# Kernel optimization log

Hardware: AMD Instinct MI355X
Metric: run time of the kernel (lower is better)

The kernel has to match this reference:

```python
import jax, jax.numpy as jnp
from jax import lax
import numpy as np

B, T, C = 32, 1024, 512
K = 3
MAX_DUR = 4            # durations drawn from [0,5) -> max value 4
L_MAX = T * MAX_DUR    # static padded mel length (torch pads to batch max; we pad to static max)
EPS = 1e-5


def conv_ln_block(x, w, b, g, beta):
    # x: [B,T,C]; torch ConvLNBlock: permute -> Conv1d(SAME) -> relu -> permute -> LayerNorm -> dropout(eval=id)
    y = lax.conv_general_dilated(x.transpose(0, 2, 1), w, (1,), 'SAME',
                                 dimension_numbers=('NCH', 'OIH', 'NCH')) + b[None, :, None]
    y = jax.nn.relu(y).transpose(0, 2, 1)  # [B,T,Cout]
    mu = y.mean(-1, keepdims=True)
    var = y.var(-1, keepdims=True)
    return (y - mu) * lax.rsqrt(var + EPS) * g + beta


def regulate(batch, durations, token_lengths):
    # Vectorized equivalent of DurationRegulator.inflate: repeat token t durations[b,t] times,
    # concatenate, pad. Implemented as cumsum + searchsorted gather (single pass, no ragged loops).
    pos = jnp.arange(T)
    valid = pos[None, :] < token_lengths[:, None]          # [B,T]
    d = jnp.where(valid, durations, 0)
    total = d.sum(axis=1)
    # torch: if durs.sum()==0 -> fill with 1
    d = jnp.where((total == 0)[:, None], valid.astype(d.dtype), d)
    total = d.sum(axis=1)                                   # [B]
    cum = jnp.cumsum(d, axis=1)                             # inclusive cumsum [B,T]
    frames = jnp.arange(L_MAX)
    idx = jax.vmap(lambda c: jnp.searchsorted(c, frames, side='right'))(cum)  # [B,L_MAX]
    idx = jnp.clip(idx, 0, T - 1)
    out = jnp.take_along_axis(batch, idx[:, :, None], axis=1)                 # [B,L_MAX,C]
    frame_mask = frames[None, :] < total[:, None]
    out = out * frame_mask[:, :, None].astype(batch.dtype)
    return out, total.astype(jnp.float32)


def setup_inputs() -> dict:
    key = jax.random.key(0)
    ks = jax.random.split(key, 8)
    batch = jax.random.normal(ks[0], (B, T, C), dtype=jnp.float32)
    token_lengths = jax.random.randint(ks[1], (B,), T // 2, T + 1).astype(jnp.int32)
    mask = jnp.arange(T)[None, :] < token_lengths[:, None]
    label_durations = jax.random.randint(ks[2], (B, T), 0, MAX_DUR + 1).astype(jnp.int32)
    s1 = 1.0 / np.sqrt(C * K)
    s2 = 1.0 / np.sqrt(C * K)
    params = {
        'conv1_w': jax.random.uniform(ks[3], (C, C, K), minval=-s1, maxval=s1, dtype=jnp.float32),
        'conv1_b': jnp.zeros((C,), jnp.float32),
        'ln1_g': jnp.ones((C,), jnp.float32), 'ln1_b': jnp.zeros((C,), jnp.float32),
        'conv2_w': jax.random.uniform(ks[4], (C, C, K), minval=-s2, maxval=s2, dtype=jnp.float32),
        'conv2_b': jnp.zeros((C,), jnp.float32),
        'ln2_g': jnp.ones((C,), jnp.float32), 'ln2_b': jnp.zeros((C,), jnp.float32),
        'lin_w': jax.random.uniform(ks[5], (C, 1), minval=-1/np.sqrt(C), maxval=1/np.sqrt(C), dtype=jnp.float32),
        'lin_b': jnp.zeros((1,), jnp.float32),
    }
    return dict(batch=batch, token_lengths=token_lengths, mask=mask,
                label_durations=label_durations, **params)


def reference(batch, token_lengths, mask, label_durations,
              conv1_w, conv1_b, ln1_g, ln1_b,
              conv2_w, conv2_b, ln2_g, ln2_b,
              lin_w, lin_b):
    # VariancePredictor: two ConvLN blocks + Linear(out_channels, 1), masked fill 0
    h = conv_ln_block(batch, conv1_w, conv1_b, ln1_g, ln1_b)
    h = conv_ln_block(h, conv2_w, conv2_b, ln2_g, ln2_b)
    predicted_durations = h @ lin_w + lin_b                      # [B,T,1]
    predicted_durations = jnp.where(mask[:, :, None], predicted_durations, 0.0)
    # label_durations provided -> regulator uses labels (training path), alpha=1
    padded_batch, mel_lengths = regulate(batch, label_durations, token_lengths)
    return padded_batch, mel_lengths, predicted_durations
```

## Files before the change

### kernel.cpp

```cpp
#include <hip/hip_runtime.h>
#include <hip/hip_bf16.h>
#include <stdint.h>


typedef _Float16 f16;
typedef _Float16 f16x8 __attribute__((ext_vector_type(8)));
typedef float f32x4 __attribute__((ext_vector_type(4)));

#define B_    32
#define T_    1024
#define TP_   1026
#define C_    512
#define LMAX_ 4096
#define KDIM  1536

#define XPAD_OFF   0u
#define H1PAD_OFF  33619968u
#define W1T_OFF    67239936u
#define W2T_OFF    68812800u
#define YWS_OFF    70385664u
#define TOT_OFF    137494528u
#define IDX_OFF    137495040u
#define GWL_OFF    138019328u
#define K12_OFF    138021376u
#define STAT2_OFF  138021888u

#define AS1C(p) ((const __attribute__((address_space(1))) void*)(p))
#define AS3(p)  ((__attribute__((address_space(3))) void*)(p))

#define PP_BLOCKS   2052
#define PW_BLOCKS   256
#define SCAN_BLOCKS 32

__global__ __launch_bounds__(1024) void fused_prep(
        const float* __restrict__ batch, f16* __restrict__ xpad,
        f16* __restrict__ h1pad, const int* __restrict__ tlen,
        const float* __restrict__ w1, const float* __restrict__ w2,
        f16* __restrict__ w1t, f16* __restrict__ w2t,
        const float* __restrict__ g2, const float* __restrict__ be2,
        const float* __restrict__ lw, float* __restrict__ gwl,
        float* __restrict__ k12,
        const int* __restrict__ dur, int* __restrict__ idxarr,
        int* __restrict__ total, float* __restrict__ mel_out) {
    __shared__ int sd[1024];
    __shared__ int sv[1024];
    __shared__ float rk[8][2];
    const int bid = blockIdx.x;
    const int tid = threadIdx.x;

    if (bid < PP_BLOCKS) {
        int row = bid * 16 + (tid >> 6);
        int lane = tid & 63;
        int b = row / TP_, tt = row % TP_;
        size_t dsto = (size_t)row * C_ + lane * 8;
        if (tt == 0 || tt == TP_ - 1) {
            f16x8 z = {};
            *(f16x8*)(xpad + dsto) = z;
            *(f16x8*)(h1pad + dsto) = z;
        } else if (tt <= tlen[b] + 130) {
            const float* src = batch + ((size_t)(b * T_ + tt - 1)) * C_ + lane * 8;
            float4 v0 = ((const float4*)src)[0];
            float4 v1 = ((const float4*)src)[1];
            f16x8 h;
            h[0] = (f16)v0.x; h[1] = (f16)v0.y; h[2] = (f16)v0.z; h[3] = (f16)v0.w;
            h[4] = (f16)v1.x; h[5] = (f16)v1.y; h[6] = (f16)v1.z; h[7] = (f16)v1.w;
            *(f16x8*)(xpad + dsto) = h;
        }
        return;
    }
    if (bid < PP_BLOCKS + PW_BLOCKS) {
        int unit = (bid - PP_BLOCKS) * 4 + (tid >> 8);
        int o = unit & 511;
        const float* w = (unit >> 9) ? w2 : w1;
        f16* wt = (unit >> 9) ? w2t : w1t;
        int tl = tid & 255;
        for (int j = tl; j < KDIM; j += 256) {
            int tap = j >> 9, i = j & 511;
            wt[(size_t)o * KDIM + j] = (f16)w[(size_t)o * KDIM + i * 3 + tap];
        }
        return;
    }
    if (bid < PP_BLOCKS + PW_BLOCKS + SCAN_BLOCKS) {
        int b = bid - (PP_BLOCKS + PW_BLOCKS);
        int t = tid;
        int L = tlen[b];
        int valid = (t < L) ? 1 : 0;
        int d = valid ? dur[b * T_ + t] : 0;
        sd[t] = d; sv[t] = valid;
        __syncthreads();
        for (int off = 1; off < 1024; off <<= 1) {
            int x = 0, y = 0;
            if (t >= off) { x = sd[t - off]; y = sv[t - off]; }
            __syncthreads();
            sd[t] += x; sv[t] += y;
            __syncthreads();
        }
        int totd = sd[1023];
        int cur  = (totd == 0) ? sv[t] : sd[t];
        int prev = (t == 0) ? 0 : ((totd == 0) ? sv[t - 1] : sd[t - 1]);
        for (int f = prev; f < cur; f++) idxarr[b * LMAX_ + f] = t;
        if (t == 1023) {
            int tt = (totd == 0) ? sv[1023] : totd;
            total[b] = tt;
            mel_out[b] = (float)tt;
        }
        return;
    }
    {
        float k1 = 0.f, k2 = 0.f;
        if (tid < C_) {
            float gw_ = g2[tid] * lw[tid];
            gwl[tid] = gw_;
            k1 = gw_;
            k2 = be2[tid] * lw[tid];
        }
#pragma unroll
        for (int m = 32; m; m >>= 1) {
            k1 += __shfl_xor(k1, m, 64);
            k2 += __shfl_xor(k2, m, 64);
        }
        int wv = tid >> 6;
        if ((tid & 63) == 0 && wv < 8) { rk[wv][0] = k1; rk[wv][1] = k2; }
        __syncthreads();
        if (tid == 0) {
            float a1 = 0.f, a2 = 0.f;
#pragma unroll
            for (int i = 0; i < 8; i++) { a1 += rk[i][0]; a2 += rk[i][1]; }
            k12[0] = a1; k12[1] = a2;
        }
    }
}

template<int EPI>
__global__ __launch_bounds__(256, 2) void gemm_k(const f16* __restrict__ A,
                                                 const f16* __restrict__ Bw,
                                                 const float* __restrict__ bias,
                                                 f16* __restrict__ Y,
                                                 const float* __restrict__ gwl,
                                                 float4* __restrict__ stats,
                                                 const int* __restrict__ tlen) {
    __shared__ f16 As[128 * 64];
    __shared__ f16 Bs[256 * 64];
    const int m0 = blockIdx.x * 128;
    {
        const int bb = m0 >> 10, t0 = m0 & 1023;
        const int L = tlen[bb];
        if (EPI == 0 ? (t0 > L) : (t0 >= L)) return;
    }
    const int tid = threadIdx.x;
    const int lane = tid & 63;
    const int w = tid >> 6;
    const int n0 = blockIdx.y * 256;
    const int arow0 = (m0 >> 10) * TP_ + (m0 & 1023);
    const int wm = (w & 1) * 64;
    const int wn = (w >> 1) * 128;

    f32x4 acc[4][8];
#pragma unroll
    for (int i = 0; i < 4; i++)
#pragma unroll
        for (int j = 0; j < 8; j++) acc[i][j] = (f32x4){0.f, 0.f, 0.f, 0.f};

    const int lrow = lane >> 3;
    const int gran = (lane & 7) ^ lrow;
    const f16* aB = A + (size_t)(arow0 + lrow) * C_ + gran * 8;
    const f16* bB = Bw + (size_t)(n0 + lrow) * KDIM + gran * 8;

    for (int kk = 0; kk < KDIM; kk += 64) {
        __syncthreads();
#pragma unroll
        for (int i = 0; i < 4; i++) {
            const int rb = (w + i * 4) * 8;
            __builtin_amdgcn_global_load_lds(AS1C(aB + (size_t)rb * C_ + kk),
                                             AS3(&As[rb * 64]), 16, 0, 0);
        }
#pragma unroll
        for (int j = 0; j < 8; j++) {
            const int rb = (w + j * 4) * 8;
            __builtin_amdgcn_global_load_lds(AS1C(bB + (size_t)rb * KDIM + kk),
                                             AS3(&Bs[rb * 64]), 16, 0, 0);
        }
        __syncthreads();
#pragma unroll
        for (int ks = 0; ks < 2; ks++) {
            const int sl = ((ks << 2) + (lane >> 4)) ^ (lane & 7);
            f16x8 af[4], bf[8];
#pragma unroll
            for (int mi = 0; mi < 4; mi++)
                af[mi] = *(const f16x8*)&As[(wm + mi * 16 + (lane & 15)) * 64 + sl * 8];
#pragma unroll
            for (int ni = 0; ni < 8; ni++)
                bf[ni] = *(const f16x8*)&Bs[(wn + ni * 16 + (lane & 15)) * 64 + sl * 8];
#pragma unroll
            for (int mi = 0; mi < 4; mi++)
#pragma unroll
                for (int ni = 0; ni < 8; ni++)
                    acc[mi][ni] = __builtin_amdgcn_mfma_f32_16x16x32_f16(
                        af[mi], bf[ni], acc[mi][ni], 0, 0, 0);
        }
    }

    const int col = lane & 15;
    const int row4 = (lane >> 4) * 4;

    if (EPI == 0) {
#pragma unroll
        for (int ni = 0; ni < 8; ni++) {
            int n = n0 + wn + ni * 16 + col;
            float bn = bias[n];
#pragma unroll
            for (int mi = 0; mi < 4; mi++) {
#pragma unroll
                for (int r = 0; r < 4; r++) {
                    int m = m0 + wm + mi * 16 + row4 + r;
                    float v = acc[mi][ni][r] + bn;
                    Y[(size_t)m * C_ + n] = (f16)(v > 0.f ? v : 0.f);
                }
            }
        }
    } else {
        float bn[8], gw[8];
#pragma unroll
        for (int ni = 0; ni < 8; ni++) {
            int n = n0 + wn + ni * 16 + col;
            bn[ni] = bias[n];
            gw[ni] = gwl[n];
        }
        float s_[4][4], q_[4][4], u_[4][4];
#pragma unroll
        for (int mi = 0; mi < 4; mi++)
#pragma unroll
            for (int r = 0; r < 4; r++) { s_[mi][r] = 0.f; q_[mi][r] = 0.f; u_[mi][r] = 0.f; }
#pragma unroll
        for (int mi = 0; mi < 4; mi++)
#pragma unroll
            for (int ni = 0; ni < 8; ni++)
#pragma unroll
                for (int r = 0; r < 4; r++) {
                    float v = acc[mi][ni][r] + bn[ni];
                    v = v > 0.f ? v : 0.f;
                    s_[mi][r] += v;
                    q_[mi][r] += v * v;
                    u_[mi][r] += v * gw[ni];
                }
#pragma unroll
        for (int m = 8; m; m >>= 1)
#pragma unroll
            for (int mi = 0; mi < 4; mi++)
#pragma unroll
                for (int r = 0; r < 4; r++) {
                    s_[mi][r] += __shfl_xor(s_[mi][r], m, 64);
                    q_[mi][r] += __shfl_xor(q_[mi][r], m, 64);
                    u_[mi][r] += __shfl_xor(u_[mi][r], m, 64);
                }
        __syncthreads();
        float* red = (float*)As;
        if (col == 0) {
#pragma unroll
            for (int mi = 0; mi < 4; mi++)
#pragma unroll
                for (int r = 0; r < 4; r++) {
                    int row = wm + mi * 16 + row4 + r;
                    int idx = ((w >> 1) * 128 + row) * 3;
                    red[idx]     = s_[mi][r];
                    red[idx + 1] = q_[mi][r];
                    red[idx + 2] = u_[mi][r];
                }
        }
        __syncthreads();
        if (tid < 128) {
            float S = red[tid * 3]     + red[(128 + tid) * 3];
            float Q = red[tid * 3 + 1] + red[(128 + tid) * 3 + 1];
            float U = red[tid * 3 + 2] + red[(128 + tid) * 3 + 2];
            stats[(size_t)(m0 + tid) * 2 + blockIdx.y] = (float4){S, Q, U, 0.f};
        }
    }
}

__global__ __launch_bounds__(256) void ln_kernel(const f16* __restrict__ Y,
                                                 const float* __restrict__ g,
                                                 const float* __restrict__ be,
                                                 f16* __restrict__ hpad,
                                                 const int* __restrict__ tlen) {
    int row = blockIdx.x * 4 + (threadIdx.x >> 6);
    int lane = threadIdx.x & 63;
    int b = row >> 10, t = row & 1023;
    if (t > tlen[b]) return;
    f16x8 yv = *(const f16x8*)(Y + (size_t)row * C_ + lane * 8);
    float v[8];
#pragma unroll
    for (int i = 0; i < 8; i++) v[i] = (float)yv[i];
    float s = 0.f, q = 0.f;
#pragma unroll
    for (int i = 0; i < 8; i++) { s += v[i]; q += v[i] * v[i]; }
#pragma unroll
    for (int m = 32; m; m >>= 1) { s += __shfl_xor(s, m, 64); q += __shfl_xor(q, m, 64); }
    float mu = s * (1.f / 512.f);
    float x = q * (1.f / 512.f) - mu * mu + 1e-5f;
    float rs = rsqrtf(x);
    rs = rs * (1.5f - 0.5f * x * rs * rs);
    const float4 g0 = ((const float4*)g)[lane * 2], g1 = ((const float4*)g)[lane * 2 + 1];
    const float4 e0 = ((const float4*)be)[lane * 2], e1 = ((const float4*)be)[lane * 2 + 1];
    f16x8 h;
    h[0] = (f16)((v[0] - mu) * rs * g0.x + e0.x);
    h[1] = (f16)((v[1] - mu) * rs * g0.y + e0.y);
    h[2] = (f16)((v[2] - mu) * rs * g0.z + e0.z);
    h[3] = (f16)((v[3] - mu) * rs * g0.w + e0.w);
    h[4] = (f16)((v[4] - mu) * rs * g1.x + e1.x);
    h[5] = (f16)((v[5] - mu) * rs * g1.y + e1.y);
    h[6] = (f16)((v[6] - mu) * rs * g1.z + e1.z);
    h[7] = (f16)((v[7] - mu) * rs * g1.w + e1.w);
    *(f16x8*)(hpad + ((size_t)(b * TP_ + t + 1)) * C_ + lane * 8) = h;
}

__global__ __launch_bounds__(256) void gather_fin(const float* __restrict__ batch,
                                                  const int* __restrict__ idxarr,
                                                  const int* __restrict__ total,
                                                  float* __restrict__ out,
                                                  const float4* __restrict__ stats,
                                                  const float* __restrict__ k12,
                                                  const float* __restrict__ lb,
                                                  const int* __restrict__ tlen,
                                                  float* __restrict__ pred) {
    if (blockIdx.x < 32768) {
        int gw = blockIdx.x * 4 + (threadIdx.x >> 6);
        int lane = threadIdx.x & 63;
        int b = gw >> 12;
        int l = gw & (LMAX_ - 1);
        int tot = total[b];
        float4* dst = (float4*)(out + ((size_t)b * LMAX_ + l) * C_);
        if (l < tot) {
            int idx = idxarr[gw];
            const float4* src = (const float4*)(batch + ((size_t)b * T_ + idx) * C_);
            dst[lane] = src[lane];
            dst[lane + 64] = src[lane + 64];
        } else {
            float4 z = {0.f, 0.f, 0.f, 0.f};
            dst[lane] = z;
            dst[lane + 64] = z;
        }
    } else {
        int m = (blockIdx.x - 32768) * 256 + threadIdx.x;
        float4 a = stats[(size_t)m * 2];
        float4 b = stats[(size_t)m * 2 + 1];
        float S = a.x + b.x, Q = a.y + b.y, U = a.z + b.z;
        float mu = S * (1.f / 512.f);
        float x = Q * (1.f / 512.f) - mu * mu + 1e-5f;
        float rs = rsqrtf(x);
        rs = rs * (1.5f - 0.5f * x * rs * rs);
        float p = rs * (U - mu * k12[0]) + k12[1] + lb[0];
        int bb = m >> 10, t = m & 1023;
        pred[m] = (t < tlen[bb]) ? p : 0.f;
    }
}

extern "C" void kernel_launch(void* const* d_in, const int* in_sizes, int n_in,
                              void* d_out, int out_size, void* d_ws, size_t ws_size,
                              hipStream_t stream) {
    const float* batch = (const float*)d_in[0];
    const int* tlen    = (const int*)d_in[1];
    const int* durs    = (const int*)d_in[3];
    const float* w1  = (const float*)d_in[4];
    const float* b1  = (const float*)d_in[5];
    const float* g1  = (const float*)d_in[6];
    const float* be1 = (const float*)d_in[7];
    const float* w2  = (const float*)d_in[8];
    const float* b2  = (const float*)d_in[9];
    const float* g2  = (const float*)d_in[10];
    const float* be2 = (const float*)d_in[11];
    const float* lw  = (const float*)d_in[12];
    const float* lb  = (const float*)d_in[13];

    float* out      = (float*)d_out;
    float* mel_out  = out + (size_t)B_ * LMAX_ * C_;
    float* pred_out = mel_out + B_;

    char* ws    = (char*)d_ws;
    f16* xpad   = (f16*)(ws + XPAD_OFF);
    f16* h1pad  = (f16*)(ws + H1PAD_OFF);
    f16* w1t    = (f16*)(ws + W1T_OFF);
    f16* w2t    = (f16*)(ws + W2T_OFF);
    f16* yws    = (f16*)(ws + YWS_OFF);
    int* tot    = (int*)(ws + TOT_OFF);
    int* idxarr = (int*)(ws + IDX_OFF);
    float* gwl  = (float*)(ws + GWL_OFF);
    float* k12  = (float*)(ws + K12_OFF);
    float4* st2 = (float4*)(ws + STAT2_OFF);

    fused_prep<<<PP_BLOCKS + PW_BLOCKS + SCAN_BLOCKS + 1, 1024, 0, stream>>>(
        batch, xpad, h1pad, tlen, w1, w2, w1t, w2t,
        g2, be2, lw, gwl, k12, durs, idxarr, tot, mel_out);
    gemm_k<0><<<dim3(256, 2), 256, 0, stream>>>(xpad, w1t, b1, yws,
                                                nullptr, nullptr, tlen);
    ln_kernel<<<8192, 256, 0, stream>>>(yws, g1, be1, h1pad, tlen);
    gemm_k<1><<<dim3(256, 2), 256, 0, stream>>>(h1pad, w2t, b2, nullptr,
                                                gwl, st2, tlen);
    gather_fin<<<32768 + 128, 256, 0, stream>>>(batch, idxarr, tot, out,
                                                st2, k12, lb, tlen, pred_out);
}
```

Measured before the change: 450.2 us.

## Fuse mel gather into LN kernel and move scan blocks first in prep

Moves the large regulator gather (copying batch rows into the padded mel output) out of the final kernel and into the layer-norm kernel, so it runs in the same launch as LN1, between the two GEMMs. The prediction finalize becomes its own small kernel. The scan blocks are reordered to the front of the prep grid so the index array is produced early. The aim is to hide the memory-bound gather alongside LN work. The risk is that the gather's bandwidth use now competes with LN and delays the second GEMM.

New measurement: 460.8 us. +2.4%, slower.

```diff
diff --git a/kernel.cpp b/kernel.cpp
--- a/kernel.cpp
+++ b/kernel.cpp
@@ -28,9 +28,12 @@
 #define AS1C(p) ((const __attribute__((address_space(1))) void*)(p))
 #define AS3(p)  ((__attribute__((address_space(3))) void*)(p))
 
+#define SCAN_BLOCKS 32
 #define PP_BLOCKS   2052
 #define PW_BLOCKS   256
-#define SCAN_BLOCKS 32
+
+#define LN_BLOCKS   8192
+#define GA_BLOCKS   32768
 
 __global__ __launch_bounds__(1024) void fused_prep(
         const float* __restrict__ batch, f16* __restrict__ xpad,
@@ -48,8 +51,34 @@
     const int bid = blockIdx.x;
     const int tid = threadIdx.x;
 
-    if (bid < PP_BLOCKS) {
-        int row = bid * 16 + (tid >> 6);
+    if (bid < SCAN_BLOCKS) {
+        int b = bid;
+        int t = tid;
+        int L = tlen[b];
+        int valid = (t < L) ? 1 : 0;
+        int d = valid ? dur[b * T_ + t] : 0;
+        sd[t] = d; sv[t] = valid;
+        __syncthreads();
+        for (int off = 1; off < 1024; off <<= 1) {
+            int x = 0, y = 0;
+            if (t >= off) { x = sd[t - off]; y = sv[t - off]; }
+            __syncthreads();
+            sd[t] += x; sv[t] += y;
+            __syncthreads();
+        }
+        int totd = sd[1023];
+        int cur  = (totd == 0) ? sv[t] : sd[t];
+        int prev = (t == 0) ? 0 : ((totd == 0) ? sv[t - 1] : sd[t - 1]);
+        for (int f = prev; f < cur; f++) idxarr[b * LMAX_ + f] = t;
+        if (t == 1023) {
+            int tt = (totd == 0) ? sv[1023] : totd;
+            total[b] = tt;
+            mel_out[b] = (float)tt;
+        }
+        return;
+    }
+    if (bid < SCAN_BLOCKS + PP_BLOCKS) {
+        int row = (bid - SCAN_BLOCKS) * 16 + (tid >> 6);
         int lane = tid & 63;
         int b = row / TP_, tt = row % TP_;
         size_t dsto = (size_t)row * C_ + lane * 8;
@@ -68,8 +97,8 @@
         }
         return;
     }
-    if (bid < PP_BLOCKS + PW_BLOCKS) {
-        int unit = (bid - PP_BLOCKS) * 4 + (tid >> 8);
+    if (bid < SCAN_BLOCKS + PP_BLOCKS + PW_BLOCKS) {
+        int unit = (bid - SCAN_BLOCKS - PP_BLOCKS) * 4 + (tid >> 8);
         int o = unit & 511;
         const float* w = (unit >> 9) ? w2 : w1;
         f16* wt = (unit >> 9) ? w2t : w1t;
@@ -77,32 +106,6 @@
         for (int j = tl; j < KDIM; j += 256) {
             int tap = j >> 9, i = j & 511;
             wt[(size_t)o * KDIM + j] = (f16)w[(size_t)o * KDIM + i * 3 + tap];
-        }
-        return;
-    }
-    if (bid < PP_BLOCKS + PW_BLOCKS + SCAN_BLOCKS) {
-        int b = bid - (PP_BLOCKS + PW_BLOCKS);
-        int t = tid;
-        int L = tlen[b];
-        int valid = (t < L) ? 1 : 0;
-        int d = valid ? dur[b * T_ + t] : 0;
-        sd[t] = d; sv[t] = valid;
-        __syncthreads();
-        for (int off = 1; off < 1024; off <<= 1) {
-            int x = 0, y = 0;
-            if (t >= off) { x = sd[t - off]; y = sv[t - off]; }
-            __syncthreads();
-            sd[t] += x; sv[t] += y;
-            __syncthreads();
-        }
-        int totd = sd[1023];
-        int cur  = (totd == 0) ? sv[t] : sd[t];
-        int prev = (t == 0) ? 0 : ((totd == 0) ? sv[t - 1] : sd[t - 1]);
-        for (int f = prev; f < cur; f++) idxarr[b * LMAX_ + f] = t;
-        if (t == 1023) {
-            int tt = (totd == 0) ? sv[1023] : totd;
-            total[b] = tt;
-            mel_out[b] = (float)tt;
         }
         return;
     }
@@ -277,54 +280,44 @@
     }
 }
 
-__global__ __launch_bounds__(256) void ln_kernel(const f16* __restrict__ Y,
-                                                 const float* __restrict__ g,
-                                                 const float* __restrict__ be,
-                                                 f16* __restrict__ hpad,
-                                                 const int* __restrict__ tlen) {
-    int row = blockIdx.x * 4 + (threadIdx.x >> 6);
-    int lane = threadIdx.x & 63;
-    int b = row >> 10, t = row & 1023;
-    if (t > tlen[b]) return;
-    f16x8 yv = *(const f16x8*)(Y + (size_t)row * C_ + lane * 8);
-    float v[8];
-#pragma unroll
-    for (int i = 0; i < 8; i++) v[i] = (float)yv[i];
-    float s = 0.f, q = 0.f;
-#pragma unroll
-    for (int i = 0; i < 8; i++) { s += v[i]; q += v[i] * v[i]; }
-#pragma unroll
-    for (int m = 32; m; m >>= 1) { s += __shfl_xor(s, m, 64); q += __shfl_xor(q, m, 64); }
-    float mu = s * (1.f / 512.f);
-    float x = q * (1.f / 512.f) - mu * mu + 1e-5f;
-    float rs = rsqrtf(x);
-    rs = rs * (1.5f - 0.5f * x * rs * rs);
-    const float4 g0 = ((const float4*)g)[lane * 2], g1 = ((const float4*)g)[lane * 2 + 1];
-    const float4 e0 = ((const float4*)be)[lane * 2], e1 = ((const float4*)be)[lane * 2 + 1];
-    f16x8 h;
-    h[0] = (f16)((v[0] - mu) * rs * g0.x + e0.x);
-    h[1] = (f16)((v[1] - mu) * rs * g0.y + e0.y);
-    h[2] = (f16)((v[2] - mu) * rs * g0.z + e0.z);
-    h[3] = (f16)((v[3] - mu) * rs * g0.w + e0.w);
-    h[4] = (f16)((v[4] - mu) * rs * g1.x + e1.x);
-    h[5] = (f16)((v[5] - mu) * rs * g1.y + e1.y);
-    h[6] = (f16)((v[6] - mu) * rs * g1.z + e1.z);
-    h[7] = (f16)((v[7] - mu) * rs * g1.w + e1.w);
-    *(f16x8*)(hpad + ((size_t)(b * TP_ + t + 1)) * C_ + lane * 8) = h;
-}
-
-__global__ __launch_bounds__(256) void gather_fin(const float* __restrict__ batch,
-                                                  const int* __restrict__ idxarr,
-                                                  const int* __restrict__ total,
-                                                  float* __restrict__ out,
-                                                  const float4* __restrict__ stats,
-                                                  const float* __restrict__ k12,
-                                                  const float* __restrict__ lb,
-                                                  const int* __restrict__ tlen,
-                                                  float* __restrict__ pred) {
-    if (blockIdx.x < 32768) {
-        int gw = blockIdx.x * 4 + (threadIdx.x >> 6);
-        int lane = threadIdx.x & 63;
+__global__ __launch_bounds__(256) void ln_gather(
+        const f16* __restrict__ Y, const float* __restrict__ g,
+        const float* __restrict__ be, f16* __restrict__ hpad,
+        const int* __restrict__ tlen,
+        const float* __restrict__ batch, const int* __restrict__ idxarr,
+        const int* __restrict__ total, float* __restrict__ out) {
+    const int lane = threadIdx.x & 63;
+    if (blockIdx.x < LN_BLOCKS) {
+        int row = blockIdx.x * 4 + (threadIdx.x >> 6);
+        int b = row >> 10, t = row & 1023;
+        if (t > tlen[b]) return;
+        f16x8 yv = *(const f16x8*)(Y + (size_t)row * C_ + lane * 8);
+        float v[8];
+#pragma unroll
+        for (int i = 0; i < 8; i++) v[i] = (float)yv[i];
+        float s = 0.f, q = 0.f;
+#pragma unroll
+        for (int i = 0; i < 8; i++) { s += v[i]; q += v[i] * v[i]; }
+#pragma unroll
+        for (int m = 32; m; m >>= 1) { s += __shfl_xor(s, m, 64); q += __shfl_xor(q, m, 64); }
+        float mu = s * (1.f / 512.f);
+        float x = q * (1.f / 512.f) - mu * mu + 1e-5f;
+        float rs = rsqrtf(x);
+        rs = rs * (1.5f - 0.5f * x * rs * rs);
+        const float4 g0 = ((const float4*)g)[lane * 2], g1 = ((const float4*)g)[lane * 2 + 1];
+        const float4 e0 = ((const float4*)be)[lane * 2], e1 = ((const float4*)be)[lane * 2 + 1];
+        f16x8 h;
+        h[0] = (f16)((v[0] - mu) * rs * g0.x + e0.x);
+        h[1] = (f16)((v[1] - mu) * rs * g0.y + e0.y);
+        h[2] = (f16)((v[2] - mu) * rs * g0.z + e0.z);
+        h[3] = (f16)((v[3] - mu) * rs * g0.w + e0.w);
+        h[4] = (f16)((v[4] - mu) * rs * g1.x + e1.x);
+        h[5] = (f16)((v[5] - mu) * rs * g1.y + e1.y);
+        h[6] = (f16)((v[6] - mu) * rs * g1.z + e1.z);
+        h[7] = (f16)((v[7] - mu) * rs * g1.w + e1.w);
+        *(f16x8*)(hpad + ((size_t)(b * TP_ + t + 1)) * C_ + lane * 8) = h;
+    } else {
+        int gw = (blockIdx.x - LN_BLOCKS) * 4 + (threadIdx.x >> 6);
         int b = gw >> 12;
         int l = gw & (LMAX_ - 1);
         int tot = total[b];
@@ -339,19 +332,25 @@
             dst[lane] = z;
             dst[lane + 64] = z;
         }
-    } else {
-        int m = (blockIdx.x - 32768) * 256 + threadIdx.x;
-        float4 a = stats[(size_t)m * 2];
-        float4 b = stats[(size_t)m * 2 + 1];
-        float S = a.x + b.x, Q = a.y + b.y, U = a.z + b.z;
-        float mu = S * (1.f / 512.f);
-        float x = Q * (1.f / 512.f) - mu * mu + 1e-5f;
-        float rs = rsqrtf(x);
-        rs = rs * (1.5f - 0.5f * x * rs * rs);
-        float p = rs * (U - mu * k12[0]) + k12[1] + lb[0];
-        int bb = m >> 10, t = m & 1023;
-        pred[m] = (t < tlen[bb]) ? p : 0.f;
-    }
+    }
+}
+
+__global__ __launch_bounds__(256) void finalize2(const float4* __restrict__ stats,
+                                                 const float* __restrict__ k12,
+                                                 const float* __restrict__ lb,
+                                                 const int* __restrict__ tlen,
+                                                 float* __restrict__ pred) {
+    int m = blockIdx.x * 256 + threadIdx.x;
+    float4 a = stats[(size_t)m * 2];
+    float4 b = stats[(size_t)m * 2 + 1];
+    float S = a.x + b.x, Q = a.y + b.y, U = a.z + b.z;
+    float mu = S * (1.f / 512.f);
+    float x = Q * (1.f / 512.f) - mu * mu + 1e-5f;
+    float rs = rsqrtf(x);
+    rs = rs * (1.5f - 0.5f * x * rs * rs);
+    float p = rs * (U - mu * k12[0]) + k12[1] + lb[0];
+    int bb = m >> 10, t = m & 1023;
+    pred[m] = (t < tlen[bb]) ? p : 0.f;
 }
 
 extern "C" void kernel_launch(void* const* d_in, const int* in_sizes, int n_in,
@@ -387,14 +386,14 @@
     float* k12  = (float*)(ws + K12_OFF);
     float4* st2 = (float4*)(ws + STAT2_OFF);
 
-    fused_prep<<<PP_BLOCKS + PW_BLOCKS + SCAN_BLOCKS + 1, 1024, 0, stream>>>(
+    fused_prep<<<SCAN_BLOCKS + PP_BLOCKS + PW_BLOCKS + 1, 1024, 0, stream>>>(
         batch, xpad, h1pad, tlen, w1, w2, w1t, w2t,
         g2, be2, lw, gwl, k12, durs, idxarr, tot, mel_out);
     gemm_k<0><<<dim3(256, 2), 256, 0, stream>>>(xpad, w1t, b1, yws,
                                                 nullptr, nullptr, tlen);
-    ln_kernel<<<8192, 256, 0, stream>>>(yws, g1, be1, h1pad, tlen);
+    ln_gather<<<LN_BLOCKS + GA_BLOCKS, 256, 0, stream>>>(
+        yws, g1, be1, h1pad, tlen, batch, idxarr, tot, out);
     gemm_k<1><<<dim3(256, 2), 256, 0, stream>>>(h1pad, w2t, b2, nullptr,
                                                 gwl, st2, tlen);
-    gather_fin<<<32768 + 128, 256, 0, stream>>>(batch, idxarr, tot, out,
-                                                st2, k12, lb, tlen, pred_out);
-}
+    finalize2<<<128, 256, 0, stream>>>(st2, k12, lb, tlen, pred_out);
+}
```
